# Kernel tuning notes

Hardware: AMD Instinct MI355X
Metric: run time of the kernel (lower is better)

## Reference

```python
import jax, jax.numpy as jnp
import numpy as np

B, T, D, DS = 8, 4096, 1024, 64


def setup_inputs() -> dict:
    key = jax.random.key(0)
    ks = jax.random.split(key, 9)
    s = 0.02
    return {
        "x": jax.random.normal(ks[0], (B, T, D), dtype=jnp.float32),
        "Wq": jax.random.normal(ks[1], (DS, D), dtype=jnp.float32) * s,
        "bq": jnp.zeros((DS,), dtype=jnp.float32),
        "Wk": jax.random.normal(ks[2], (DS, D), dtype=jnp.float32) * s,
        "bk": jnp.zeros((DS,), dtype=jnp.float32),
        "Wv": jax.random.normal(ks[3], (DS, D), dtype=jnp.float32) * s,
        "bv": jnp.zeros((DS,), dtype=jnp.float32),
        "decay": jnp.full((DS,), 0.95, dtype=jnp.float32),
        "Wo": jax.random.normal(ks[4], (D, DS), dtype=jnp.float32) * s,
        "bo": jnp.zeros((D,), dtype=jnp.float32),
    }


def reference(x, Wq, bq, Wk, bk, Wv, bv, decay, Wo, bo):
    # projections: [B,T,DS]
    q = jnp.einsum('btd,sd->bts', x, Wq) + bq
    k = jnp.einsum('btd,sd->bts', x, Wk) + bk
    v = jnp.einsum('btd,sd->bts', x, Wv) + bv
    d = jax.nn.sigmoid(decay)  # [DS]

    def step(S, qkv_t):
        q_t, k_t, v_t = qkv_t  # each [B, DS]
        # diag(d) @ S + v k^T  (rank-1 update per batch)
        S = d[None, :, None] * S + v_t[:, :, None] * k_t[:, None, :]
        o = jnp.einsum('bij,bj->bi', S, q_t)
        return S, o

    S0 = jnp.zeros((x.shape[0], d.shape[0], d.shape[0]), dtype=x.dtype)
    qkv = (jnp.swapaxes(q, 0, 1), jnp.swapaxes(k, 0, 1), jnp.swapaxes(v, 0, 1))  # [T,B,DS]
    _, outs = jax.lax.scan(step, S0, qkv)  # outs: [T,B,DS]
    scan_out = jnp.swapaxes(outs, 0, 1)  # [B,T,DS]
    return x + jnp.einsum('bts,ds->btd', scan_out, Wo) + bo
```

## Files before the change

### kernel.cpp

```cpp
#include <hip/hip_runtime.h>
#include <cstdint>
#include <cstddef>
#include <cmath>

#define Bb 8
#define Tt 4096
#define Dd 1024
#define DS 64
#define Mm (Bb*Tt)
#define PAD 68

typedef __bf16 bf16x8 __attribute__((ext_vector_type(8)));
typedef __bf16 bf16x4v __attribute__((ext_vector_type(4)));
typedef float f32x4 __attribute__((ext_vector_type(4)));

__device__ __forceinline__ float4* ldsP(float* buf, int row, int col4) {
  return (float4*)(buf + row * PAD + (((col4) ^ ((row >> 3) & 7)) << 2));
}

__global__ __launch_bounds__(256) void convert_w(
    const float* __restrict__ Wq, const float* __restrict__ Wk,
    const float* __restrict__ Wv, const float* __restrict__ Wo,
    __bf16* __restrict__ Wqkvb, __bf16* __restrict__ Wob)
{
  int idx = blockIdx.x * 256 + threadIdx.x;
  if (idx < 196608) {
    float v = (idx < 65536) ? Wq[idx]
            : (idx < 131072) ? Wk[idx - 65536] : Wv[idx - 131072];
    Wqkvb[idx] = (__bf16)v;
  }
  if (idx < 65536) Wob[idx] = (__bf16)Wo[idx];
}

__global__ __launch_bounds__(256) void qkv_mfma(
    const float* __restrict__ x, const __bf16* __restrict__ Wb,
    const float* __restrict__ bq, const float* __restrict__ bk,
    const float* __restrict__ bv, float* __restrict__ qkv)
{
  __shared__ __bf16 xs[64 * 64];

  const int tid = threadIdx.x;
  const int w   = tid >> 6;
  const int l   = tid & 63;
  const int m0  = blockIdx.x * 64;
  const int c0  = w * 48;
  const int lr  = l & 15;
  const int lk  = l >> 4;

  const int srow = tid & 63;
  const int sk   = (tid >> 6) * 16;
  const float* xsrc = x + (size_t)(m0 + srow) * 1024 + sk;
  const int wb0 = srow * 128 + ((sk * 2 + 0)  ^ ((srow & 7) << 4));
  const int wb1 = srow * 128 + ((sk * 2 + 16) ^ ((srow & 7) << 4));

  f32x4 acc[3][4] = {};

  float4 f0 = *(const float4*)(xsrc + 0);
  float4 f1 = *(const float4*)(xsrc + 4);
  float4 f2 = *(const float4*)(xsrc + 8);
  float4 f3 = *(const float4*)(xsrc + 12);

  for (int k0 = 0; k0 < 1024; k0 += 64) {
    bf16x8 h0, h1;
    h0[0] = (__bf16)f0.x; h0[1] = (__bf16)f0.y; h0[2] = (__bf16)f0.z; h0[3] = (__bf16)f0.w;
    h0[4] = (__bf16)f1.x; h0[5] = (__bf16)f1.y; h0[6] = (__bf16)f1.z; h0[7] = (__bf16)f1.w;
    h1[0] = (__bf16)f2.x; h1[1] = (__bf16)f2.y; h1[2] = (__bf16)f2.z; h1[3] = (__bf16)f2.w;
    h1[4] = (__bf16)f3.x; h1[5] = (__bf16)f3.y; h1[6] = (__bf16)f3.z; h1[7] = (__bf16)f3.w;

    __syncthreads();
    *(bf16x8*)((char*)xs + wb0) = h0;
    *(bf16x8*)((char*)xs + wb1) = h1;
    __syncthreads();

    if (k0 + 64 < 1024) {
      f0 = *(const float4*)(xsrc + k0 + 64);
      f1 = *(const float4*)(xsrc + k0 + 68);
      f2 = *(const float4*)(xsrc + k0 + 72);
      f3 = *(const float4*)(xsrc + k0 + 76);
    }

    #pragma unroll
    for (int ks = 0; ks < 2; ++ks) {
      bf16x8 wf[3], xf[4];
      #pragma unroll
      for (int jf = 0; jf < 3; ++jf)
        wf[jf] = *(const bf16x8*)(Wb + (size_t)(c0 + jf * 16 + lr) * 1024
                                     + k0 + ks * 32 + lk * 8);
      #pragma unroll
      for (int mf = 0; mf < 4; ++mf) {
        int row = mf * 16 + lr;
        int boff = row * 128 + ((ks * 64 + lk * 16) ^ ((row & 7) << 4));
        xf[mf] = *(const bf16x8*)((const char*)xs + boff);
      }
      #pragma unroll
      for (int jf = 0; jf < 3; ++jf)
        #pragma unroll
        for (int mf = 0; mf < 4; ++mf)
          acc[jf][mf] = __builtin_amdgcn_mfma_f32_16x16x32_bf16(
              wf[jf], xf[mf], acc[jf][mf], 0, 0, 0);
    }
  }

  #pragma unroll
  for (int jf = 0; jf < 3; ++jf) {
    int j0 = c0 + jf * 16 + lk * 4;
    const float* bsrc = (j0 < 64) ? (bq + j0)
                      : (j0 < 128) ? (bk + j0 - 64) : (bv + j0 - 128);
    float4 b4 = *(const float4*)bsrc;
    #pragma unroll
    for (int mf = 0; mf < 4; ++mf) {
      int m = m0 + mf * 16 + lr;
      float4 o;
      o.x = acc[jf][mf][0] + b4.x;
      o.y = acc[jf][mf][1] + b4.y;
      o.z = acc[jf][mf][2] + b4.z;
      o.w = acc[jf][mf][3] + b4.w;
      *(float4*)(qkv + (size_t)m * 192 + j0) = o;
    }
  }
}

__global__ __launch_bounds__(256) void scan_chunk_a(
    const float* __restrict__ qkv, const float* __restrict__ decay,
    float* __restrict__ Ubuf, float* __restrict__ so)
{
  __shared__ float Qs[64 * PAD];
  __shared__ float Ks[64 * PAD];
  __shared__ float Vs[64 * PAD];
  __shared__ float l2d[64];

  const int tid = threadIdx.x;
  const int bc  = blockIdx.x;
  const int b   = bc >> 6;
  const int ch  = bc & 63;
  const int ti  = tid >> 4;
  const int tj  = tid & 15;

  const float* base = qkv + ((size_t)(b * Tt + ch * 64)) * 192;

  #pragma unroll
  for (int it = 0; it < 12; ++it) {
    int idx = tid + it * 256;
    int row = idx / 48, f = idx % 48;
    float4 g = *(const float4*)(base + (size_t)row * 192 + f * 4);
    float4* dst;
    if (f < 16)      dst = ldsP(Qs, row, f);
    else if (f < 32) dst = ldsP(Ks, row, f - 16);
    else             dst = ldsP(Vs, row, f - 32);
    *dst = g;
  }
  if (tid < 64) {
    float d = 1.0f / (1.0f + expf(-decay[tid]));
    l2d[tid] = log2f(d);
  }
  __syncthreads();

  {
    int s = tid >> 2;
    #pragma unroll
    for (int g4 = 0; g4 < 4; ++g4) {
      int col4 = (tid & 3) * 4 + g4;
      float4* p = ldsP(Vs, s, col4);
      float4 v = *p;
      float e0 = exp2f(-(float)s * l2d[col4 * 4 + 0]);
      float e1 = exp2f(-(float)s * l2d[col4 * 4 + 1]);
      float e2 = exp2f(-(float)s * l2d[col4 * 4 + 2]);
      float e3 = exp2f(-(float)s * l2d[col4 * 4 + 3]);
      v.x *= e0; v.y *= e1; v.z *= e2; v.w *= e3;
      *p = v;
    }
  }

  float gval[4][4] = {};
  #pragma unroll
  for (int kk4 = 0; kk4 < 16; ++kk4) {
    float4 K4[4], Q4[4];
    #pragma unroll
    for (int r = 0; r < 4; ++r) K4[r] = *ldsP(Ks, ti * 4 + r, kk4);
    #pragma unroll
    for (int c = 0; c < 4; ++c) Q4[c] = *ldsP(Qs, tj * 4 + c, kk4);
    #pragma unroll
    for (int r = 0; r < 4; ++r)
      #pragma unroll
      for (int c = 0; c < 4; ++c) {
        gval[r][c] = fmaf(K4[r].x, Q4[c].x, gval[r][c]);
        gval[r][c] = fmaf(K4[r].y, Q4[c].y, gval[r][c]);
        gval[r][c] = fmaf(K4[r].z, Q4[c].z, gval[r][c]);
        gval[r][c] = fmaf(K4[r].w, Q4[c].w, gval[r][c]);
      }
  }
  #pragma unroll
  for (int r = 0; r < 4; ++r)
    #pragma unroll
    for (int c = 0; c < 4; ++c)
      if (ti * 4 + r > tj * 4 + c) gval[r][c] = 0.0f;

  __syncthreads();

  #pragma unroll
  for (int r = 0; r < 4; ++r) {
    float4 g4 = {gval[r][0], gval[r][1], gval[r][2], gval[r][3]};
    *ldsP(Qs, ti * 4 + r, tj) = g4;
  }
  __syncthreads();

  float uacc[4][4] = {};
  float oacc[4][4] = {};
  for (int s = 0; s < 64; ++s) {
    float4 Vti = *ldsP(Vs, s, ti);
    float4 Ktj = *ldsP(Ks, s, tj);
    float4 Gti = *ldsP(Qs, s, ti);
    float4 Vtj = *ldsP(Vs, s, tj);
    const float vi[4] = {Vti.x, Vti.y, Vti.z, Vti.w};
    const float kj[4] = {Ktj.x, Ktj.y, Ktj.z, Ktj.w};
    const float gu[4] = {Gti.x, Gti.y, Gti.z, Gti.w};
    const float vj[4] = {Vtj.x, Vtj.y, Vtj.z, Vtj.w};
    #pragma unroll
    for (int r = 0; r < 4; ++r)
      #pragma unroll
      for (int c = 0; c < 4; ++c) {
        uacc[r][c] = fmaf(vi[r], kj[c], uacc[r][c]);
        oacc[r][c] = fmaf(gu[r], vj[c], oacc[r][c]);
      }
  }

  #pragma unroll
  for (int r = 0; r < 4; ++r) {
    int i = ti * 4 + r;
    float d63 = exp2f(63.0f * l2d[i]);
    float4 o = {uacc[r][0] * d63, uacc[r][1] * d63,
                uacc[r][2] * d63, uacc[r][3] * d63};
    *(float4*)(Ubuf + ((size_t)bc * 64 + i) * 64 + tj * 4) = o;
  }
  #pragma unroll
  for (int r = 0; r < 4; ++r) {
    int u = ti * 4 + r;
    float e0 = exp2f((float)u * l2d[tj * 4 + 0]);
    float e1 = exp2f((float)u * l2d[tj * 4 + 1]);
    float e2 = exp2f((float)u * l2d[tj * 4 + 2]);
    float e3 = exp2f((float)u * l2d[tj * 4 + 3]);
    float4 o = {oacc[r][0] * e0, oacc[r][1] * e1,
                oacc[r][2] * e2, oacc[r][3] * e3};
    *(float4*)(so + ((size_t)(b * Tt + ch * 64 + u)) * 64 + tj * 4) = o;
  }
}

__global__ __launch_bounds__(256) void scan_state(
    const float* __restrict__ decay, float* __restrict__ Ubuf)
{
  const int b  = blockIdx.x >> 2;
  const int jq = blockIdx.x & 3;
  const int i  = threadIdx.x >> 2;
  const int j4 = threadIdx.x & 3;

  float d = 1.0f / (1.0f + expf(-decay[i]));
  float d2 = d * d, d4 = d2 * d2, d8 = d4 * d4;
  float d16 = d8 * d8, d32 = d16 * d16, d64 = d32 * d32;

  float* base = Ubuf + ((size_t)b * 64) * 4096 + (size_t)i * 64 + jq * 16 + j4 * 4;

  float4 S = {0.f, 0.f, 0.f, 0.f};
  float4 u0 = *(const float4*)(base + 0 * 4096);
  float4 u1 = *(const float4*)(base + 1 * 4096);
  float4 u2 = *(const float4*)(base + 2 * 4096);
  float4 u3 = *(const float4*)(base + 3 * 4096);

  for (int c = 0; c < 64; c += 4) {
    float4 n0 = u0, n1 = u1, n2 = u2, n3 = u3;
    if (c + 4 < 64) {
      n0 = *(const float4*)(base + (size_t)(c + 4) * 4096);
      n1 = *(const float4*)(base + (size_t)(c + 5) * 4096);
      n2 = *(const float4*)(base + (size_t)(c + 6) * 4096);
      n3 = *(const float4*)(base + (size_t)(c + 7) * 4096);
    }
    *(float4*)(base + (size_t)(c + 0) * 4096) = S;
    S.x = fmaf(d64, S.x, u0.x); S.y = fmaf(d64, S.y, u0.y);
    S.z = fmaf(d64, S.z, u0.z); S.w = fmaf(d64, S.w, u0.w);
    *(float4*)(base + (size_t)(c + 1) * 4096) = S;
    S.x = fmaf(d64, S.x, u1.x); S.y = fmaf(d64, S.y, u1.y);
    S.z = fmaf(d64, S.z, u1.z); S.w = fmaf(d64, S.w, u1.w);
    *(float4*)(base + (size_t)(c + 2) * 4096) = S;
    S.x = fmaf(d64, S.x, u2.x); S.y = fmaf(d64, S.y, u2.y);
    S.z = fmaf(d64, S.z, u2.z); S.w = fmaf(d64, S.w, u2.w);
    *(float4*)(base + (size_t)(c + 3) * 4096) = S;
    S.x = fmaf(d64, S.x, u3.x); S.y = fmaf(d64, S.y, u3.y);
    S.z = fmaf(d64, S.z, u3.z); S.w = fmaf(d64, S.w, u3.w);
    u0 = n0; u1 = n1; u2 = n2; u3 = n3;
  }
}

__global__ __launch_bounds__(256) void scan_chunk_c(
    const float* __restrict__ qkv, const float* __restrict__ decay,
    const float* __restrict__ Sbuf, const float* __restrict__ so,
    __bf16* __restrict__ sob)
{
  __shared__ float Ss[64 * PAD];
  __shared__ float Qs[64 * PAD];
  __shared__ float l2d[64];

  const int tid = threadIdx.x;
  const int bc  = blockIdx.x;
  const int b   = bc >> 6;
  const int ch  = bc & 63;
  const int ti  = tid >> 4;
  const int tj  = tid & 15;

  #pragma unroll
  for (int it = 0; it < 4; ++it) {
    int idx = tid + it * 256;
    int row = idx >> 4, col4 = idx & 15;
    float4 s4 = *(const float4*)(Sbuf + (size_t)bc * 4096 + (size_t)row * 64 + col4 * 4);
    *ldsP(Ss, row, col4) = s4;
    float4 q4 = *(const float4*)(qkv + ((size_t)(b * Tt + ch * 64 + row)) * 192 + col4 * 4);
    *ldsP(Qs, row, col4) = q4;
  }
  if (tid < 64) {
    float d = 1.0f / (1.0f + expf(-decay[tid]));
    l2d[tid] = log2f(d);
  }
  __syncthreads();

  float acc[4][4] = {};
  #pragma unroll
  for (int j4 = 0; j4 < 16; ++j4) {
    float4 Q4[4], S4[4];
    #pragma unroll
    for (int r = 0; r < 4; ++r) Q4[r] = *ldsP(Qs, ti * 4 + r, j4);
    #pragma unroll
    for (int c = 0; c < 4; ++c) S4[c] = *ldsP(Ss, tj * 4 + c, j4);
    #pragma unroll
    for (int r = 0; r < 4; ++r)
      #pragma unroll
      for (int c = 0; c < 4; ++c) {
        acc[r][c] = fmaf(Q4[r].x, S4[c].x, acc[r][c]);
        acc[r][c] = fmaf(Q4[r].y, S4[c].y, acc[r][c]);
        acc[r][c] = fmaf(Q4[r].z, S4[c].z, acc[r][c]);
        acc[r][c] = fmaf(Q4[r].w, S4[c].w, acc[r][c]);
      }
  }

  #pragma unroll
  for (int r = 0; r < 4; ++r) {
    int u = ti * 4 + r;
    size_t row = (size_t)(b * Tt + ch * 64 + u);
    float4 prev = *(const float4*)(so + row * 64 + tj * 4);
    float e0 = exp2f((float)(u + 1) * l2d[tj * 4 + 0]);
    float e1 = exp2f((float)(u + 1) * l2d[tj * 4 + 1]);
    float e2 = exp2f((float)(u + 1) * l2d[tj * 4 + 2]);
    float e3 = exp2f((float)(u + 1) * l2d[tj * 4 + 3]);
    bf16x4v ov;
    ov[0] = (__bf16)fmaf(acc[r][0], e0, prev.x);
    ov[1] = (__bf16)fmaf(acc[r][1], e1, prev.y);
    ov[2] = (__bf16)fmaf(acc[r][2], e2, prev.z);
    ov[3] = (__bf16)fmaf(acc[r][3], e3, prev.w);
    *(bf16x4v*)(sob + row * 64 + tj * 4) = ov;
  }
}

__global__ __launch_bounds__(256) void out_mfma(
    const float* __restrict__ x, const __bf16* __restrict__ sob,
    const __bf16* __restrict__ Wob, const float* __restrict__ bo,
    float* __restrict__ out)
{
  const int bid = blockIdx.x;
  const int rb  = bid >> 3;
  const int cb  = bid & 7;
  const int w   = threadIdx.x >> 6;
  const int l   = threadIdx.x & 63;
  const int wr  = w >> 1;
  const int wc  = w & 1;
  const int m0  = rb * 128 + wr * 64;
  const int c0  = cb * 128 + wc * 64;
  const int lr  = l & 15;
  const int lk  = l >> 4;

  f32x4 acc[4][4] = {};

  const __bf16* ap = Wob + (size_t)(c0 + lr) * 64 + lk * 8;
  const __bf16* bp = sob + (size_t)(m0 + lr) * 64 + lk * 8;

  #pragma unroll
  for (int ks = 0; ks < 2; ++ks) {
    bf16x8 a[4], b[4];
    #pragma unroll
    for (int jf = 0; jf < 4; ++jf)
      a[jf] = *(const bf16x8*)(ap + (size_t)jf * 16 * 64 + ks * 32);
    #pragma unroll
    for (int mf = 0; mf < 4; ++mf)
      b[mf] = *(const bf16x8*)(bp + (size_t)mf * 16 * 64 + ks * 32);
    #pragma unroll
    for (int jf = 0; jf < 4; ++jf)
      #pragma unroll
      for (int mf = 0; mf < 4; ++mf)
        acc[jf][mf] = __builtin_amdgcn_mfma_f32_16x16x32_bf16(
            a[jf], b[mf], acc[jf][mf], 0, 0, 0);
  }

  #pragma unroll
  for (int jf = 0; jf < 4; ++jf) {
    int j0 = c0 + jf * 16 + lk * 4;
    float4 b4 = *(const float4*)(bo + j0);
    #pragma unroll
    for (int mf = 0; mf < 4; ++mf) {
      size_t m = (size_t)m0 + mf * 16 + lr;
      float4 xv = *(const float4*)(x + m * 1024 + j0);
      float4 o;
      o.x = xv.x + acc[jf][mf][0] + b4.x;
      o.y = xv.y + acc[jf][mf][1] + b4.y;
      o.z = xv.z + acc[jf][mf][2] + b4.z;
      o.w = xv.w + acc[jf][mf][3] + b4.w;
      *(float4*)(out + m * 1024 + j0) = o;
    }
  }
}

extern "C" void kernel_launch(void* const* d_in, const int* in_sizes, int n_in,
                              void* d_out, int out_size, void* d_ws, size_t ws_size,
                              hipStream_t stream)
{
  const float* x   = (const float*)d_in[0];
  const float* Wq  = (const float*)d_in[1];
  const float* bq  = (const float*)d_in[2];
  const float* Wk  = (const float*)d_in[3];
  const float* bk  = (const float*)d_in[4];
  const float* Wv  = (const float*)d_in[5];
  const float* bv  = (const float*)d_in[6];
  const float* dec = (const float*)d_in[7];
  const float* Wo  = (const float*)d_in[8];
  const float* bo  = (const float*)d_in[9];
  float* out = (float*)d_out;

  float*  qkv   = (float*)d_ws;
  float*  so    = qkv + (size_t)Mm * 192;
  float*  Ubuf  = so + (size_t)Mm * 64;
  __bf16* sob   = (__bf16*)(Ubuf + (size_t)512 * 4096);
  __bf16* Wqkvb = sob + (size_t)Mm * 64;
  __bf16* Wob   = Wqkvb + (size_t)192 * 1024;

  convert_w<<<768, 256, 0, stream>>>(Wq, Wk, Wv, Wo, Wqkvb, Wob);
  qkv_mfma<<<Mm / 64, 256, 0, stream>>>(x, Wqkvb, bq, bk, bv, qkv);
  scan_chunk_a<<<512, 256, 0, stream>>>(qkv, dec, Ubuf, so);
  scan_state<<<32, 256, 0, stream>>>(dec, Ubuf);
  scan_chunk_c<<<512, 256, 0, stream>>>(qkv, dec, Ubuf, so, sob);
  out_mfma<<<2048, 256, 0, stream>>>(x, sob, Wob, bo, out);
}
```

Baseline: 388.7 us.

## Coalesce x loads in QKV GEMM, restage out GEMM through LDS, widen scan_state grid

After: 368.7 us. -5.2%, faster.

```diff
diff --git a/kernel.cpp b/kernel.cpp
--- a/kernel.cpp
+++ b/kernel.cpp
@@ -47,36 +47,37 @@
   const int lr  = l & 15;
   const int lk  = l >> 4;
 
-  const int srow = tid & 63;
-  const int sk   = (tid >> 6) * 16;
-  const float* xsrc = x + (size_t)(m0 + srow) * 1024 + sk;
-  const int wb0 = srow * 128 + ((sk * 2 + 0)  ^ ((srow & 7) << 4));
-  const int wb1 = srow * 128 + ((sk * 2 + 16) ^ ((srow & 7) << 4));
+  const int sr0 = tid >> 4;
+  const int sc4 = tid & 15;
+  const float* xsrc = x + (size_t)(m0 + sr0) * 1024 + sc4 * 4;
 
   f32x4 acc[3][4] = {};
 
-  float4 f0 = *(const float4*)(xsrc + 0);
-  float4 f1 = *(const float4*)(xsrc + 4);
-  float4 f2 = *(const float4*)(xsrc + 8);
-  float4 f3 = *(const float4*)(xsrc + 12);
+  float4 f[4];
+  #pragma unroll
+  for (int g = 0; g < 4; ++g)
+    f[g] = *(const float4*)(xsrc + (size_t)g * 16 * 1024);
 
   for (int k0 = 0; k0 < 1024; k0 += 64) {
-    bf16x8 h0, h1;
-    h0[0] = (__bf16)f0.x; h0[1] = (__bf16)f0.y; h0[2] = (__bf16)f0.z; h0[3] = (__bf16)f0.w;
-    h0[4] = (__bf16)f1.x; h0[5] = (__bf16)f1.y; h0[6] = (__bf16)f1.z; h0[7] = (__bf16)f1.w;
-    h1[0] = (__bf16)f2.x; h1[1] = (__bf16)f2.y; h1[2] = (__bf16)f2.z; h1[3] = (__bf16)f2.w;
-    h1[4] = (__bf16)f3.x; h1[5] = (__bf16)f3.y; h1[6] = (__bf16)f3.z; h1[7] = (__bf16)f3.w;
+    bf16x4v h[4];
+    #pragma unroll
+    for (int g = 0; g < 4; ++g) {
+      h[g][0] = (__bf16)f[g].x; h[g][1] = (__bf16)f[g].y;
+      h[g][2] = (__bf16)f[g].z; h[g][3] = (__bf16)f[g].w;
+    }
 
     __syncthreads();
-    *(bf16x8*)((char*)xs + wb0) = h0;
-    *(bf16x8*)((char*)xs + wb1) = h1;
+    #pragma unroll
+    for (int g = 0; g < 4; ++g) {
+      int row = sr0 + 16 * g;
+      *(bf16x4v*)((char*)xs + row * 128 + ((sc4 * 8) ^ ((row & 7) << 4))) = h[g];
+    }
     __syncthreads();
 
     if (k0 + 64 < 1024) {
-      f0 = *(const float4*)(xsrc + k0 + 64);
-      f1 = *(const float4*)(xsrc + k0 + 68);
-      f2 = *(const float4*)(xsrc + k0 + 72);
-      f3 = *(const float4*)(xsrc + k0 + 76);
+      #pragma unroll
+      for (int g = 0; g < 4; ++g)
+        f[g] = *(const float4*)(xsrc + (size_t)g * 16 * 1024 + k0 + 64);
     }
 
     #pragma unroll
@@ -245,19 +246,18 @@
   }
 }
 
-__global__ __launch_bounds__(256) void scan_state(
+__global__ __launch_bounds__(64) void scan_state(
     const float* __restrict__ decay, float* __restrict__ Ubuf)
 {
-  const int b  = blockIdx.x >> 2;
-  const int jq = blockIdx.x & 3;
-  const int i  = threadIdx.x >> 2;
-  const int j4 = threadIdx.x & 3;
+  const int b  = blockIdx.x >> 4;
+  const int jq = blockIdx.x & 15;
+  const int i  = threadIdx.x;
 
   float d = 1.0f / (1.0f + expf(-decay[i]));
   float d2 = d * d, d4 = d2 * d2, d8 = d4 * d4;
   float d16 = d8 * d8, d32 = d16 * d16, d64 = d32 * d32;
 
-  float* base = Ubuf + ((size_t)b * 64) * 4096 + (size_t)i * 64 + jq * 16 + j4 * 4;
+  float* base = Ubuf + ((size_t)b * 64) * 4096 + (size_t)i * 64 + jq * 4;
 
   float4 S = {0.f, 0.f, 0.f, 0.f};
   float4 u0 = *(const float4*)(base + 0 * 4096);
@@ -362,54 +362,61 @@
     const __bf16* __restrict__ Wob, const float* __restrict__ bo,
     float* __restrict__ out)
 {
-  const int bid = blockIdx.x;
-  const int rb  = bid >> 3;
-  const int cb  = bid & 7;
-  const int w   = threadIdx.x >> 6;
-  const int l   = threadIdx.x & 63;
-  const int wr  = w >> 1;
-  const int wc  = w & 1;
-  const int m0  = rb * 128 + wr * 64;
-  const int c0  = cb * 128 + wc * 64;
-  const int lr  = l & 15;
-  const int lk  = l >> 4;
-
-  f32x4 acc[4][4] = {};
-
-  const __bf16* ap = Wob + (size_t)(c0 + lr) * 64 + lk * 8;
+  __shared__ float ps[4][16 * 64];
+
+  const int w  = threadIdx.x >> 6;
+  const int l  = threadIdx.x & 63;
+  const int lr = l & 15;
+  const int lk = l >> 4;
+  const int m0 = blockIdx.x * 64 + w * 16;
+  const int er = l >> 4;
+  const int ec = l & 15;
+
   const __bf16* bp = sob + (size_t)(m0 + lr) * 64 + lk * 8;
-
-  #pragma unroll
-  for (int ks = 0; ks < 2; ++ks) {
-    bf16x8 a[4], b[4];
-    #pragma unroll
-    for (int jf = 0; jf < 4; ++jf)
-      a[jf] = *(const bf16x8*)(ap + (size_t)jf * 16 * 64 + ks * 32);
-    #pragma unroll
-    for (int mf = 0; mf < 4; ++mf)
-      b[mf] = *(const bf16x8*)(bp + (size_t)mf * 16 * 64 + ks * 32);
-    #pragma unroll
-    for (int jf = 0; jf < 4; ++jf)
-      #pragma unroll
-      for (int mf = 0; mf < 4; ++mf)
-        acc[jf][mf] = __builtin_amdgcn_mfma_f32_16x16x32_bf16(
-            a[jf], b[mf], acc[jf][mf], 0, 0, 0);
-  }
-
-  #pragma unroll
-  for (int jf = 0; jf < 4; ++jf) {
-    int j0 = c0 + jf * 16 + lk * 4;
-    float4 b4 = *(const float4*)(bo + j0);
-    #pragma unroll
-    for (int mf = 0; mf < 4; ++mf) {
-      size_t m = (size_t)m0 + mf * 16 + lr;
-      float4 xv = *(const float4*)(x + m * 1024 + j0);
+  bf16x8 bf0 = *(const bf16x8*)(bp);
+  bf16x8 bf1 = *(const bf16x8*)(bp + 32);
+
+  float* myps = ps[w];
+
+  for (int jblk = 0; jblk < 16; ++jblk) {
+    const int j0 = jblk * 64;
+
+    float4 xv[4];
+    #pragma unroll
+    for (int k = 0; k < 4; ++k)
+      xv[k] = *(const float4*)(x + (size_t)(m0 + er + 4 * k) * 1024 + j0 + ec * 4);
+    float4 b4 = *(const float4*)(bo + j0 + ec * 4);
+
+    const __bf16* ap = Wob + (size_t)(j0 + lr) * 64 + lk * 8;
+    f32x4 acc[4];
+    #pragma unroll
+    for (int jf = 0; jf < 4; ++jf) {
+      bf16x8 a0 = *(const bf16x8*)(ap + (size_t)jf * 16 * 64);
+      bf16x8 a1 = *(const bf16x8*)(ap + (size_t)jf * 16 * 64 + 32);
+      f32x4 t = {0.f, 0.f, 0.f, 0.f};
+      t = __builtin_amdgcn_mfma_f32_16x16x32_bf16(a0, bf0, t, 0, 0, 0);
+      t = __builtin_amdgcn_mfma_f32_16x16x32_bf16(a1, bf1, t, 0, 0, 0);
+      acc[jf] = t;
+    }
+
+    #pragma unroll
+    for (int jf = 0; jf < 4; ++jf) {
+      int c4 = jf * 4 + lk;
+      float4 v = {acc[jf][0], acc[jf][1], acc[jf][2], acc[jf][3]};
+      *(float4*)((char*)myps + lr * 256 + ((c4 * 16) ^ ((lr & 7) << 4))) = v;
+    }
+
+    #pragma unroll
+    for (int k = 0; k < 4; ++k) {
+      int r = er + 4 * k;
+      float4 pv = *(const float4*)((char*)myps + r * 256 + ((ec * 16) ^ ((r & 7) << 4)));
+      size_t m = (size_t)(m0 + r);
       float4 o;
-      o.x = xv.x + acc[jf][mf][0] + b4.x;
-      o.y = xv.y + acc[jf][mf][1] + b4.y;
-      o.z = xv.z + acc[jf][mf][2] + b4.z;
-      o.w = xv.w + acc[jf][mf][3] + b4.w;
-      *(float4*)(out + m * 1024 + j0) = o;
+      o.x = xv[k].x + pv.x + b4.x;
+      o.y = xv[k].y + pv.y + b4.y;
+      o.z = xv[k].z + pv.z + b4.z;
+      o.w = xv[k].w + pv.w + b4.w;
+      *(float4*)(out + m * 1024 + j0 + ec * 4) = o;
     }
   }
 }
@@ -440,7 +447,7 @@
   convert_w<<<768, 256, 0, stream>>>(Wq, Wk, Wv, Wo, Wqkvb, Wob);
   qkv_mfma<<<Mm / 64, 256, 0, stream>>>(x, Wqkvb, bq, bk, bv, qkv);
   scan_chunk_a<<<512, 256, 0, stream>>>(qkv, dec, Ubuf, so);
-  scan_state<<<32, 256, 0, stream>>>(dec, Ubuf);
+  scan_state<<<128, 64, 0, stream>>>(dec, Ubuf);
   scan_chunk_c<<<512, 256, 0, stream>>>(qkv, dec, Ubuf, so, sob);
-  out_mfma<<<2048, 256, 0, stream>>>(x, sob, Wob, bo, out);
-}
+  out_mfma<<<512, 256, 0, stream>>>(x, sob, Wob, bo, out);
+}
```
